# Performance work log

Measured on AMD Instinct MI355X. Metric: run time of the kernel, lower is better.

Reference implementation:

```python
import jax, jax.numpy as jnp
import numpy as np

N = 50000   # nodes
E = 800000  # edges
C = 64      # node feature channels (0e)
A = 4       # edge attr channels
B = 16      # edge embedding (radial basis) size
H = 8       # radial MLP hidden size
D = 32      # query/key channels
P = 16      # node attr channels
R_MAX = 5.0


def setup_inputs() -> dict:
    key = jax.random.key(0)
    ks = jax.random.split(key, 20)
    w = lambda k, shape, fan_in: (jax.random.normal(k, shape, jnp.float32) / np.sqrt(fan_in).astype(np.float32))
    inp = {
        "node_feats": jax.random.normal(ks[0], (N, C), jnp.float32),
        "node_attrs": jax.random.normal(ks[1], (N, P), jnp.float32),
        "edge_embedding": jax.random.uniform(ks[2], (E, B), jnp.float32),
        "edge_attrs": jax.random.normal(ks[3], (E, A), jnp.float32),
        "positions": jax.random.normal(ks[4], (N, 3), jnp.float32) * 0.3,  # keep lengths < r_max
        "edge_src": jax.random.randint(ks[5], (E,), 0, N),
        "edge_dst": jax.random.randint(ks[6], (E,), 0, N),
        # parameters
        "W_q": w(ks[7], (C, D), C),            # h_q Linear
        "W1_k": w(ks[8], (B, H), B),           # radial MLP for tp_k
        "W2_k": w(ks[9], (H, C * A), H),
        "W1_v": w(ks[10], (B, H), B),          # radial MLP for tp_v
        "W2_v": w(ks[11], (H, C * A), H),
        "W_lin_k": w(ks[12], (C, D), C),       # linear_k
        "W_lin_v": w(ks[13], (C, C), C),       # linear_v
        "W_dot": w(ks[14], (D, D), D * D),     # FullyConnectedTensorProduct(q,k,'0e')
        "W_sc": w(ks[15], (C, P, C), C * P),   # self connection FCTP
    }
    return inp


def soft_unit_step(x):
    safe = jnp.where(x > 0, x, 1.0)
    return jnp.where(x > 0, jnp.exp(-1.0 / safe), 0.0)


def uvu_tp(x_src, edge_attrs, edge_embedding, W1, W2):
    # radial MLP -> per-edge, per-path weights [E, C, A]; 'uvu' tensor product on scalars
    wgt = (jax.nn.silu(edge_embedding @ W1) @ W2).reshape(-1, C, A)
    return x_src * (jnp.einsum('eca,ea->ec', wgt, edge_attrs) / np.sqrt(A).astype(np.float32))


def reference(node_feats, node_attrs, edge_embedding, edge_attrs, positions,
              edge_src, edge_dst, W_q, W1_k, W2_k, W1_v, W2_v,
              W_lin_k, W_lin_v, W_dot, W_sc):
    q = (node_feats @ W_q)[edge_dst]                              # [E, D]
    x_src = node_feats[edge_src]                                  # [E, C]
    k = uvu_tp(x_src, edge_attrs, edge_embedding, W1_k, W2_k) @ W_lin_k  # [E, D]
    v = uvu_tp(x_src, edge_attrs, edge_embedding, W1_v, W2_v) @ W_lin_v  # [E, C]

    edge_vec = positions[edge_dst] - positions[edge_src]
    edge_length = jnp.linalg.norm(edge_vec, axis=1)               # [E]
    cutoff = soft_unit_step(2.0 * R_MAX * (1.0 - edge_length / R_MAX))

    score = jnp.einsum('ei,ij,ej->e', q, W_dot, k)                # weighted bilinear dot -> 0e
    expv = cutoff * jnp.exp(score)                                # [E]
    z = jax.ops.segment_sum(expv, edge_dst, num_segments=N)       # softmax normalizer
    z = jnp.where(z == 0, 1.0, z)
    alpha = expv / z[edge_dst]
    msg = jnp.sqrt(jax.nn.relu(alpha))[:, None] * v               # [E, C]
    node_out = jax.ops.segment_sum(msg, edge_dst, num_segments=N)  # [N, C]

    sc = jnp.einsum('nc,np,cpo->no', node_feats, node_attrs, W_sc)
    return node_out + sc
```

## Files before the change

kernel.cpp:

```cpp
#include <hip/hip_runtime.h>
#include <math.h>

#define NN 50000
#define EE 800000
#define NPAD 50176

typedef __attribute__((ext_vector_type(8))) short short8v;
typedef __attribute__((ext_vector_type(4))) float f32x4;

static __device__ __forceinline__ short bf16r(float x) {
  union { float f; unsigned u; } v; v.f = x;
  unsigned r = v.u + 0x7FFFu + ((v.u >> 16) & 1u);
  return (short)(r >> 16);
}
static __device__ __forceinline__ float bf2f(unsigned u) {
  union { unsigned u; float f; } v; v.u = u << 16;
  return v.f;
}
static __device__ __forceinline__ unsigned pk2(float a, float b) {
  return (unsigned)(unsigned short)bf16r(a) | ((unsigned)(unsigned short)bf16r(b) << 16);
}


__global__ __launch_bounds__(256) void prep_kernel(
    const float* __restrict__ Wq, const float* __restrict__ Wdot,
    const float* __restrict__ Wlk, const float* __restrict__ W2k,
    const float* __restrict__ W2v, const float* __restrict__ Wlv,
    const float* __restrict__ Wsc, float* __restrict__ M,
    unsigned short* __restrict__ w2kT, unsigned short* __restrict__ w2vT,
    unsigned short* __restrict__ wlvb, unsigned short* __restrict__ wscb,
    int* __restrict__ cur, int* __restrict__ bsum)
{
  const int tid = threadIdx.x;
  const int b = blockIdx.x;
  if (b == 0) {
    __shared__ float tmp[2048];
#pragma unroll
    for (int r = 0; r < 8; ++r) {
      int idx = tid + r * 256;
      int cin = idx >> 5, d = idx & 31;
      float a = 0.f;
      for (int j = 0; j < 32; ++j) a = fmaf(Wq[cin * 32 + j], Wdot[j * 32 + d], a);
      tmp[idx] = a;
    }
    __syncthreads();
#pragma unroll
    for (int r = 0; r < 16; ++r) {
      int idx = tid + r * 256;
      int cin = idx >> 6, c = idx & 63;
      float a = 0.f;
      for (int d = 0; d < 32; ++d) a = fmaf(tmp[cin * 32 + d], Wlk[c * 32 + d], a);
      M[idx] = a;
    }
#pragma unroll
    for (int r = 0; r < 8; ++r) {
      int idx = tid + r * 256;
      int c = idx >> 5, k = idx & 31, h = k >> 2, a = k & 3;
      w2kT[idx] = (unsigned short)bf16r(W2k[h * 256 + c * 4 + a]);
      w2vT[idx] = (unsigned short)bf16r(W2v[h * 256 + c * 4 + a]);
    }
#pragma unroll
    for (int r = 0; r < 16; ++r) {
      int idx = tid + r * 256;
      int o = idx >> 6, c = idx & 63;
      wlvb[idx] = (unsigned short)bf16r(Wlv[c * 64 + o]);
    }
  } else if (b <= 196) {
    cur[(b - 1) * 256 + tid] = 0;
    if (b == 1 && tid == 0) bsum[255] = 0;
  } else {
    int w = (b - 197) * 256 + tid;
    int c = w & 63, o = (w >> 6) & 63, p = w >> 12;
    wscb[w] = (unsigned short)bf16r(Wsc[c * 1024 + p * 64 + o]);
  }
}

__global__ __launch_bounds__(256) void tqhist_kernel(
    const float* __restrict__ nf, const float* __restrict__ M,
    const int* __restrict__ edst, int* __restrict__ cur,
    float4* __restrict__ zu,
    unsigned short* __restrict__ tqb, unsigned short* __restrict__ nfb)
{
  __shared__ float Ml[4096];
  __shared__ float nfl[64 * 68];
  const int tid = threadIdx.x;
  if (blockIdx.x < 3125) {
    int i = blockIdx.x * 256 + tid;
    float4 zf = make_float4(0.f, 0.f, 0.f, 0.f);
    zu[i] = zf;
    if (i < 12544) zu[800000 + i] = zf;
    atomicAdd(&cur[edst[i]], 1);
    return;
  }
  const int base = (blockIdx.x - 3125) * 64;
#pragma unroll
  for (int r = 0; r < 4; ++r) {
    int idx = tid + r * 256;
    reinterpret_cast<float4*>(Ml)[idx] = reinterpret_cast<const float4*>(M)[idx];
  }
#pragma unroll
  for (int r = 0; r < 4; ++r) {
    int idx = tid + r * 256;
    int row = idx >> 4, c4 = idx & 15;
    float4 v = make_float4(0.f, 0.f, 0.f, 0.f);
    if (base + row < NN) v = reinterpret_cast<const float4*>(nf)[(base + row) * 16 + c4];
    *reinterpret_cast<float4*>(&nfl[row * 68 + c4 * 4]) = v;
  }
  __syncthreads();
  const int to = tid & 15, tn = tid >> 4;
  float4 acc[4] = {make_float4(0,0,0,0), make_float4(0,0,0,0),
                   make_float4(0,0,0,0), make_float4(0,0,0,0)};
  for (int c = 0; c < 64; ++c) {
    float4 m = reinterpret_cast<const float4*>(Ml)[c * 16 + to];
#pragma unroll
    for (int i = 0; i < 4; ++i) {
      float x = nfl[(tn * 4 + i) * 68 + c];
      acc[i].x = fmaf(x, m.x, acc[i].x);
      acc[i].y = fmaf(x, m.y, acc[i].y);
      acc[i].z = fmaf(x, m.z, acc[i].z);
      acc[i].w = fmaf(x, m.w, acc[i].w);
    }
  }
#pragma unroll
  for (int i = 0; i < 4; ++i) {
    int n = base + tn * 4 + i;
    if (n < NN) {
      unsigned* tp = reinterpret_cast<unsigned*>(tqb) + (size_t)n * 32 + to * 2;
      tp[0] = pk2(acc[i].x, acc[i].y);
      tp[1] = pk2(acc[i].z, acc[i].w);
    }
  }
#pragma unroll
  for (int r = 0; r < 8; ++r) {
    int idx = tid + r * 256;
    int row = idx >> 5, cp = idx & 31;
    int n = base + row;
    if (n < NN) {
      reinterpret_cast<unsigned*>(nfb)[(size_t)n * 32 + cp] =
          pk2(nfl[row * 68 + cp * 2], nfl[row * 68 + cp * 2 + 1]);
    }
  }
}

__global__ __launch_bounds__(256) void scanAB_kernel(
    int* __restrict__ cur, int* __restrict__ bsum)
{
  __shared__ int s[256];
  __shared__ int isLast;
  const int tid = threadIdx.x;
  const int i = blockIdx.x * 256 + tid;
  int v = cur[i];
  s[tid] = v;
  __syncthreads();
  for (int off = 1; off < 256; off <<= 1) {
    int t = (tid >= off) ? s[tid - off] : 0;
    __syncthreads();
    s[tid] += t;
    __syncthreads();
  }
  cur[i] = s[tid] - v;
  if (tid == 255) bsum[blockIdx.x] = s[255];
  __threadfence();
  if (tid == 0) isLast = (atomicAdd(&bsum[255], 1) == 195);
  __syncthreads();
  if (!isLast) return;
  int v2 = (tid < 196) ? atomicAdd(&bsum[tid], 0) : 0;
  s[tid] = v2;
  __syncthreads();
  for (int off = 1; off < 256; off <<= 1) {
    int t = (tid >= off) ? s[tid - off] : 0;
    __syncthreads();
    s[tid] += t;
    __syncthreads();
  }
  if (tid < 196) bsum[tid] = s[tid] - v2;
}

__global__ __launch_bounds__(256) void scatter_fused(
    const int* __restrict__ esrc, const int* __restrict__ edst,
    const float* __restrict__ ea, const float* __restrict__ eb,
    const float* __restrict__ pos, const float* __restrict__ W1k,
    const float* __restrict__ W1v, int* __restrict__ cur,
    const int* __restrict__ bsum, int* __restrict__ perm,
    float* __restrict__ rec)
{
  int e = blockIdx.x * 256 + threadIdx.x;
  int s = esrc[e], d = edst[e];
  int r = atomicAdd(&cur[d], 1) + bsum[d >> 8];
  perm[r] = e;
  float dx = pos[d * 3 + 0] - pos[s * 3 + 0];
  float dy = pos[d * 3 + 1] - pos[s * 3 + 1];
  float dz = pos[d * 3 + 2] - pos[s * 3 + 2];
  float len = sqrtf(fmaf(dx, dx, fmaf(dy, dy, dz * dz)));
  float arg = 10.f - 2.f * len;
  float cl = (arg > 0.f) ? __expf(-1.f / arg) : 0.f;
  const f32x4* eb4 = reinterpret_cast<const f32x4*>(eb);
  f32x4 q0 = eb4[e * 4 + 0], q1 = eb4[e * 4 + 1],
        q2 = eb4[e * 4 + 2], q3 = eb4[e * 4 + 3];
  float ebv[16] = {q0.x, q0.y, q0.z, q0.w, q1.x, q1.y, q1.z, q1.w,
                   q2.x, q2.y, q2.z, q2.w, q3.x, q3.y, q3.z, q3.w};
  float h[16];
#pragma unroll
  for (int j = 0; j < 16; ++j) h[j] = 0.f;
#pragma unroll
  for (int b = 0; b < 16; ++b) {
    float x = ebv[b];
#pragma unroll
    for (int j = 0; j < 8; ++j) {
      h[j]     = fmaf(x, W1k[b * 8 + j], h[j]);
      h[8 + j] = fmaf(x, W1v[b * 8 + j], h[8 + j]);
    }
  }
#pragma unroll
  for (int j = 0; j < 16; ++j) h[j] = h[j] / (1.f + __expf(-h[j]));

  f32x4 a4 = reinterpret_cast<const f32x4*>(ea)[e];
  f32x4* rp4 = reinterpret_cast<f32x4*>(rec + (size_t)e * 12);
  f32x4 w0, w1, w2;
  w0.x = cl;
  w0.y = __uint_as_float(pk2(a4.x, a4.y));
  w0.z = __uint_as_float(pk2(a4.z, a4.w));
  w0.w = 0.f;
  w1.x = __uint_as_float(pk2(h[0], h[1]));
  w1.y = __uint_as_float(pk2(h[8], h[9]));
  w1.z = __uint_as_float(pk2(h[2], h[3]));
  w1.w = __uint_as_float(pk2(h[10], h[11]));
  w2.x = __uint_as_float(pk2(h[4], h[5]));
  w2.y = __uint_as_float(pk2(h[12], h[13]));
  w2.z = __uint_as_float(pk2(h[6], h[7]));
  w2.w = __uint_as_float(pk2(h[14], h[15]));
  rp4[0] = w0;
  rp4[1] = w1;
  rp4[2] = w2;
}

__global__ __launch_bounds__(256) void edge_kernel(
    const unsigned short* __restrict__ nfb, const unsigned short* __restrict__ tqb,
    const float* __restrict__ rec, const int* __restrict__ perm,
    const int* __restrict__ esrc, const int* __restrict__ edst,
    const unsigned short* __restrict__ w2kT, const unsigned short* __restrict__ w2vT,
    float* __restrict__ z, float* __restrict__ U)
{
  __shared__ float xsAll[4][16 * 68];
  __shared__ int   esAll[4][16];
  __shared__ int   edAll[4][16];
  __shared__ float clAll[4][16];
  __shared__ float evAll[4][16];
  const int tid  = threadIdx.x;
  const int lane = tid & 63;
  const int w = tid >> 6;
  const int lo = lane & 15, hi = lane >> 4;
  const int sb = (blockIdx.x * 4 + w) * 16;
  float* xs = xsAll[w];
  int*   es = esAll[w];
  int*   ed = edAll[w];
  float* cl = clAll[w];
  float* evs = evAll[w];

  short8v bk[4], bv[4];
#pragma unroll
  for (int t = 0; t < 4; ++t) {
    bk[t] = *reinterpret_cast<const short8v*>(&w2kT[(16 * t + lo) * 32 + hi * 8]);
    bv[t] = *reinterpret_cast<const short8v*>(&w2vT[(16 * t + lo) * 32 + hi * 8]);
  }

  const int eL = perm[sb + lo];
  const unsigned* ru = reinterpret_cast<const unsigned*>(rec);
  const size_t rb = (size_t)eL * 12;
  unsigned ea01 = ru[rb + 1];
  unsigned ea23 = ru[rb + 2];
  uint2 kv = *reinterpret_cast<const uint2*>(&ru[rb + 4 + 2 * hi]);
  unsigned k01 = kv.x, v01 = kv.y;
  if (hi == 0) {
    es[lo] = esrc[eL];
    ed[lo] = edst[eL];
    cl[lo] = rec[rb];
  }
  __builtin_amdgcn_wave_barrier();

#pragma unroll
  for (int r = 0; r < 2; ++r) {
    int idx = lane + r * 64;
    int e = idx >> 3, c8 = idx & 7;
    float4 pv = reinterpret_cast<const float4*>(nfb)[(size_t)es[e] * 8 + c8];
    unsigned u0 = __float_as_uint(pv.x), u1 = __float_as_uint(pv.y),
             u2 = __float_as_uint(pv.z), u3 = __float_as_uint(pv.w);
    float* xp = &xs[e * 68 + c8 * 8];
    xp[0] = bf2f(u0 & 0xffffu); xp[1] = bf2f(u0 >> 16);
    xp[2] = bf2f(u1 & 0xffffu); xp[3] = bf2f(u1 >> 16);
    xp[4] = bf2f(u2 & 0xffffu); xp[5] = bf2f(u2 >> 16);
    xp[6] = bf2f(u3 & 0xffffu); xp[7] = bf2f(u3 >> 16);
  }

  float ax = bf2f(ea01 & 0xffffu), ay = bf2f(ea01 >> 16);
  float az = bf2f(ea23 & 0xffffu), aw = bf2f(ea23 >> 16);
  float hk0 = bf2f(k01 & 0xffffu), hk1 = bf2f(k01 >> 16);
  float hv0 = bf2f(v01 & 0xffffu), hv1 = bf2f(v01 >> 16);
  short8v ak, av;
  ak[0] = bf16r(hk0 * ax); ak[1] = bf16r(hk0 * ay);
  ak[2] = bf16r(hk0 * az); ak[3] = bf16r(hk0 * aw);
  ak[4] = bf16r(hk1 * ax); ak[5] = bf16r(hk1 * ay);
  ak[6] = bf16r(hk1 * az); ak[7] = bf16r(hk1 * aw);
  av[0] = bf16r(hv0 * ax); av[1] = bf16r(hv0 * ay);
  av[2] = bf16r(hv0 * az); av[3] = bf16r(hv0 * aw);
  av[4] = bf16r(hv1 * ax); av[5] = bf16r(hv1 * ay);
  av[6] = bf16r(hv1 * az); av[7] = bf16r(hv1 * aw);
  __builtin_amdgcn_wave_barrier();

  f32x4 zero = {0.f, 0.f, 0.f, 0.f};
  f32x4 ack[4], acv[4];
#pragma unroll
  for (int t = 0; t < 4; ++t) {
    ack[t] = __builtin_amdgcn_mfma_f32_16x16x32_bf16(ak, bk[t], zero, 0, 0, 0);
    acv[t] = __builtin_amdgcn_mfma_f32_16x16x32_bf16(av, bv[t], zero, 0, 0, 0);
  }

  const int erow = 4 * hi;
  const unsigned short* tp0 = tqb + (size_t)ed[erow + 0] * 64;
  const unsigned short* tp1 = tqb + (size_t)ed[erow + 1] * 64;
  const unsigned short* tp2 = tqb + (size_t)ed[erow + 2] * 64;
  const unsigned short* tp3 = tqb + (size_t)ed[erow + 3] * 64;
  float p0 = 0.f, p1 = 0.f, p2 = 0.f, p3 = 0.f;
#pragma unroll
  for (int t = 0; t < 4; ++t) {
    int c = lo + 16 * t;
    p0 = fmaf(xs[(erow + 0) * 68 + c] * bf2f(tp0[c]), ack[t][0], p0);
    p1 = fmaf(xs[(erow + 1) * 68 + c] * bf2f(tp1[c]), ack[t][1], p1);
    p2 = fmaf(xs[(erow + 2) * 68 + c] * bf2f(tp2[c]), ack[t][2], p2);
    p3 = fmaf(xs[(erow + 3) * 68 + c] * bf2f(tp3[c]), ack[t][3], p3);
  }
#pragma unroll
  for (int off = 1; off < 16; off <<= 1) {
    p0 += __shfl_xor(p0, off);
    p1 += __shfl_xor(p1, off);
    p2 += __shfl_xor(p2, off);
    p3 += __shfl_xor(p3, off);
  }
  float ev0 = cl[erow + 0] * __expf(0.5f * p0);
  float ev1 = cl[erow + 1] * __expf(0.5f * p1);
  float ev2 = cl[erow + 2] * __expf(0.5f * p2);
  float ev3 = cl[erow + 3] * __expf(0.5f * p3);
  float se0 = sqrtf(ev0), se1 = sqrtf(ev1), se2 = sqrtf(ev2), se3 = sqrtf(ev3);
  if (lo < 4) {
    float ev = (lo == 0) ? ev0 : (lo == 1) ? ev1 : (lo == 2) ? ev2 : ev3;
    evs[erow + lo] = ev;
  }
#pragma unroll
  for (int i = 0; i < 4; ++i) {
    const float se = (i == 0) ? se0 : (i == 1) ? se1 : (i == 2) ? se2 : se3;
    float* xr = &xs[(erow + i) * 68 + lo];
#pragma unroll
    for (int t = 0; t < 4; ++t) {
      xr[16 * t] = se * xr[16 * t] * acv[t][i];
    }
  }
  __builtin_amdgcn_wave_barrier();
  {
    const int c = lane;
    float acc = 0.f, evacc = 0.f;
    int prev = ed[0];
#pragma unroll
    for (int r = 0; r < 16; ++r) {
      int d = ed[r];
      if (d != prev) {
        unsafeAtomicAdd(&U[prev * 64 + c], acc);
        if (c == 0) unsafeAtomicAdd(&z[prev], evacc);
        acc = 0.f; evacc = 0.f; prev = d;
      }
      acc += xs[r * 68 + c];
      if (c == 0) evacc += evs[r];
    }
    unsafeAtomicAdd(&U[prev * 64 + c], acc);
    if (c == 0) unsafeAtomicAdd(&z[prev], evacc);
  }
}

__global__ __launch_bounds__(256, 4) void final_kernel(
    const float* __restrict__ nf, const float* __restrict__ na,
    const float* __restrict__ U, const float* __restrict__ z,
    const unsigned short* __restrict__ wscb, const unsigned short* __restrict__ wlvb,
    float* __restrict__ out)
{
  __shared__ float nfl[64 * 68];
  __shared__ float Ul[64 * 68];
  __shared__ float nal[64 * 17];
  __shared__ float sl[64];
  const int tid = threadIdx.x;
  const int lane = tid & 63;
  const int lo = lane & 15, hi = lane >> 4;
  const int w = tid >> 6;
  const int nb = blockIdx.x * 64;

#pragma unroll
  for (int r = 0; r < 4; ++r) {
    int idx = tid + r * 256;
    int row = idx >> 4, c4 = idx & 15;
    int n = nb + row; if (n >= NN) n = NN - 1;
    float4 v = reinterpret_cast<const float4*>(nf)[n * 16 + c4];
    *reinterpret_cast<float4*>(&nfl[row * 68 + c4 * 4]) = v;
    float4 u = reinterpret_cast<const float4*>(U)[n * 16 + c4];
    *reinterpret_cast<float4*>(&Ul[row * 68 + c4 * 4]) = u;
  }
#pragma unroll
  for (int r = 0; r < 4; ++r) {
    int idx = tid + r * 256;
    int row = idx >> 4, p = idx & 15;
    int n = nb + row; if (n >= NN) n = NN - 1;
    nal[row * 17 + p] = na[n * 16 + p];
  }
  if (tid < 64) {
    int n = nb + tid; if (n >= NN) n = NN - 1;
    float zz = z[n];
    sl[tid] = (zz > 0.f) ? 0.5f * rsqrtf(zz) : 0.f;
  }
  __syncthreads();

  const int row = 16 * w + lo;
  short8v anf[2], au[2];
#pragma unroll
  for (int kk = 0; kk < 2; ++kk) {
#pragma unroll
    for (int j = 0; j < 8; ++j) {
      anf[kk][j] = bf16r(nfl[row * 68 + 32 * kk + 8 * hi + j]);
      au[kk][j]  = bf16r(Ul[row * 68 + 32 * kk + 8 * hi + j]);
    }
  }

  f32x4 zeroA = {0.f, 0.f, 0.f, 0.f};
  f32x4 accS[4] = {zeroA, zeroA, zeroA, zeroA};
  f32x4 accU[4] = {zeroA, zeroA, zeroA, zeroA};

#pragma unroll
  for (int t = 0; t < 4; ++t) {
    short8v b0 = *reinterpret_cast<const short8v*>(&wlvb[(16 * t + lo) * 64 + 8 * hi]);
    short8v b1 = *reinterpret_cast<const short8v*>(&wlvb[(16 * t + lo) * 64 + 32 + 8 * hi]);
    accU[t] = __builtin_amdgcn_mfma_f32_16x16x32_bf16(au[0], b0, accU[t], 0, 0, 0);
    accU[t] = __builtin_amdgcn_mfma_f32_16x16x32_bf16(au[1], b1, accU[t], 0, 0, 0);
  }
#pragma unroll 1
  for (int p = 0; p < 16; ++p) {
    f32x4 cp[4] = {zeroA, zeroA, zeroA, zeroA};
#pragma unroll
    for (int t = 0; t < 4; ++t) {
      const int bbase = (p * 64 + 16 * t + lo) * 64 + 8 * hi;
      short8v b0 = *reinterpret_cast<const short8v*>(&wscb[bbase]);
      short8v b1 = *reinterpret_cast<const short8v*>(&wscb[bbase + 32]);
      cp[t] = __builtin_amdgcn_mfma_f32_16x16x32_bf16(anf[0], b0, cp[t], 0, 0, 0);
      cp[t] = __builtin_amdgcn_mfma_f32_16x16x32_bf16(anf[1], b1, cp[t], 0, 0, 0);
    }
#pragma unroll
    for (int i = 0; i < 4; ++i) {
      float nav = nal[(16 * w + 4 * hi + i) * 17 + p];
#pragma unroll
      for (int t = 0; t < 4; ++t) accS[t][i] = fmaf(nav, cp[t][i], accS[t][i]);
    }
  }
#pragma unroll
  for (int i = 0; i < 4; ++i) {
    int n = nb + 16 * w + 4 * hi + i;
    if (n < NN) {
      float s = sl[16 * w + 4 * hi + i];
#pragma unroll
      for (int t = 0; t < 4; ++t) {
        out[n * 64 + 16 * t + lo] = fmaf(s, accU[t][i], accS[t][i]);
      }
    }
  }
}

extern "C" void kernel_launch(void* const* d_in, const int* in_sizes, int n_in,
                              void* d_out, int out_size, void* d_ws, size_t ws_size,
                              hipStream_t stream) {
  const float* nf   = (const float*)d_in[0];
  const float* na   = (const float*)d_in[1];
  const float* eb   = (const float*)d_in[2];
  const float* ea   = (const float*)d_in[3];
  const float* pos  = (const float*)d_in[4];
  const int*   esrc = (const int*)d_in[5];
  const int*   edst = (const int*)d_in[6];
  const float* Wq   = (const float*)d_in[7];
  const float* W1k  = (const float*)d_in[8];
  const float* W2k  = (const float*)d_in[9];
  const float* W1v  = (const float*)d_in[10];
  const float* W2v  = (const float*)d_in[11];
  const float* Wlk  = (const float*)d_in[12];
  const float* Wlv  = (const float*)d_in[13];
  const float* Wdot = (const float*)d_in[14];
  const float* Wsc  = (const float*)d_in[15];
  float* out = (float*)d_out;

  float* wsf = (float*)d_ws;
  float* z    = wsf;
  float* U    = wsf + 50176;
  unsigned short* nfb = (unsigned short*)(wsf + 3250176);
  unsigned short* tqb = (unsigned short*)(wsf + 4850176);
  unsigned short* w2kT = (unsigned short*)(wsf + 6450176);
  unsigned short* w2vT = (unsigned short*)(wsf + 6451200);
  unsigned short* wlvb = (unsigned short*)(wsf + 6452224);
  unsigned short* wscb = (unsigned short*)(wsf + 6454272);
  int*   cur  = (int*)(wsf + 6487040);
  int*   bsum = (int*)(wsf + 6537216);
  float* M    = wsf + 6537472;
  float* rec  = wsf + 6541568;
  int*   perm = (int*)(wsf + 16141568);

  prep_kernel<<<453, 256, 0, stream>>>(Wq, Wdot, Wlk, W2k, W2v, Wlv, Wsc,
                                       M, w2kT, w2vT, wlvb, wscb, cur, bsum);
  tqhist_kernel<<<3907, 256, 0, stream>>>(nf, M, edst, cur, (float4*)z, tqb, nfb);
  scanAB_kernel<<<196, 256, 0, stream>>>(cur, bsum);
  scatter_fused<<<EE / 256, 256, 0, stream>>>(esrc, edst, ea, eb, pos, W1k, W1v,
                                              cur, bsum, perm, rec);
  edge_kernel<<<EE / 64, 256, 0, stream>>>(nfb, tqb, rec, perm, esrc, edst,
                                           w2kT, w2vT, z, U);
  final_kernel<<<(NN + 63) / 64, 256, 0, stream>>>(nf, na, U, z, wscb, wlvb, out);
}
```

Before: 314.4 us.

## Fuse radial MLP and cutoff into edge kernel, drop packed edge record

```diff
diff --git a/kernel.cpp b/kernel.cpp
--- a/kernel.cpp
+++ b/kernel.cpp
@@ -176,68 +176,22 @@
   if (tid < 196) bsum[tid] = s[tid] - v2;
 }
 
-__global__ __launch_bounds__(256) void scatter_fused(
-    const int* __restrict__ esrc, const int* __restrict__ edst,
-    const float* __restrict__ ea, const float* __restrict__ eb,
-    const float* __restrict__ pos, const float* __restrict__ W1k,
-    const float* __restrict__ W1v, int* __restrict__ cur,
-    const int* __restrict__ bsum, int* __restrict__ perm,
-    float* __restrict__ rec)
+__global__ __launch_bounds__(256) void perm_scatter(
+    const int* __restrict__ edst, int* __restrict__ cur,
+    const int* __restrict__ bsum, int* __restrict__ perm)
 {
   int e = blockIdx.x * 256 + threadIdx.x;
-  int s = esrc[e], d = edst[e];
+  int d = edst[e];
   int r = atomicAdd(&cur[d], 1) + bsum[d >> 8];
   perm[r] = e;
-  float dx = pos[d * 3 + 0] - pos[s * 3 + 0];
-  float dy = pos[d * 3 + 1] - pos[s * 3 + 1];
-  float dz = pos[d * 3 + 2] - pos[s * 3 + 2];
-  float len = sqrtf(fmaf(dx, dx, fmaf(dy, dy, dz * dz)));
-  float arg = 10.f - 2.f * len;
-  float cl = (arg > 0.f) ? __expf(-1.f / arg) : 0.f;
-  const f32x4* eb4 = reinterpret_cast<const f32x4*>(eb);
-  f32x4 q0 = eb4[e * 4 + 0], q1 = eb4[e * 4 + 1],
-        q2 = eb4[e * 4 + 2], q3 = eb4[e * 4 + 3];
-  float ebv[16] = {q0.x, q0.y, q0.z, q0.w, q1.x, q1.y, q1.z, q1.w,
-                   q2.x, q2.y, q2.z, q2.w, q3.x, q3.y, q3.z, q3.w};
-  float h[16];
-#pragma unroll
-  for (int j = 0; j < 16; ++j) h[j] = 0.f;
-#pragma unroll
-  for (int b = 0; b < 16; ++b) {
-    float x = ebv[b];
-#pragma unroll
-    for (int j = 0; j < 8; ++j) {
-      h[j]     = fmaf(x, W1k[b * 8 + j], h[j]);
-      h[8 + j] = fmaf(x, W1v[b * 8 + j], h[8 + j]);
-    }
-  }
-#pragma unroll
-  for (int j = 0; j < 16; ++j) h[j] = h[j] / (1.f + __expf(-h[j]));
-
-  f32x4 a4 = reinterpret_cast<const f32x4*>(ea)[e];
-  f32x4* rp4 = reinterpret_cast<f32x4*>(rec + (size_t)e * 12);
-  f32x4 w0, w1, w2;
-  w0.x = cl;
-  w0.y = __uint_as_float(pk2(a4.x, a4.y));
-  w0.z = __uint_as_float(pk2(a4.z, a4.w));
-  w0.w = 0.f;
-  w1.x = __uint_as_float(pk2(h[0], h[1]));
-  w1.y = __uint_as_float(pk2(h[8], h[9]));
-  w1.z = __uint_as_float(pk2(h[2], h[3]));
-  w1.w = __uint_as_float(pk2(h[10], h[11]));
-  w2.x = __uint_as_float(pk2(h[4], h[5]));
-  w2.y = __uint_as_float(pk2(h[12], h[13]));
-  w2.z = __uint_as_float(pk2(h[6], h[7]));
-  w2.w = __uint_as_float(pk2(h[14], h[15]));
-  rp4[0] = w0;
-  rp4[1] = w1;
-  rp4[2] = w2;
 }
 
 __global__ __launch_bounds__(256) void edge_kernel(
     const unsigned short* __restrict__ nfb, const unsigned short* __restrict__ tqb,
-    const float* __restrict__ rec, const int* __restrict__ perm,
-    const int* __restrict__ esrc, const int* __restrict__ edst,
+    const int* __restrict__ perm, const int* __restrict__ esrc,
+    const int* __restrict__ edst, const float* __restrict__ ea,
+    const float* __restrict__ eb, const float* __restrict__ pos,
+    const float* __restrict__ W1k, const float* __restrict__ W1v,
     const unsigned short* __restrict__ w2kT, const unsigned short* __restrict__ w2vT,
     float* __restrict__ z, float* __restrict__ U)
 {
@@ -265,16 +219,16 @@
   }
 
   const int eL = perm[sb + lo];
-  const unsigned* ru = reinterpret_cast<const unsigned*>(rec);
-  const size_t rb = (size_t)eL * 12;
-  unsigned ea01 = ru[rb + 1];
-  unsigned ea23 = ru[rb + 2];
-  uint2 kv = *reinterpret_cast<const uint2*>(&ru[rb + 4 + 2 * hi]);
-  unsigned k01 = kv.x, v01 = kv.y;
+  const f32x4* eb4 = reinterpret_cast<const f32x4*>(eb);
+  f32x4 q0 = eb4[(size_t)eL * 4 + 0], q1 = eb4[(size_t)eL * 4 + 1],
+        q2 = eb4[(size_t)eL * 4 + 2], q3 = eb4[(size_t)eL * 4 + 3];
+  f32x4 a4 = reinterpret_cast<const f32x4*>(ea)[eL];
+  int sN = 0, dN = 0;
   if (hi == 0) {
-    es[lo] = esrc[eL];
-    ed[lo] = edst[eL];
-    cl[lo] = rec[rb];
+    sN = esrc[eL];
+    dN = edst[eL];
+    es[lo] = sN;
+    ed[lo] = dN;
   }
   __builtin_amdgcn_wave_barrier();
 
@@ -292,19 +246,40 @@
     xp[6] = bf2f(u3 & 0xffffu); xp[7] = bf2f(u3 >> 16);
   }
 
-  float ax = bf2f(ea01 & 0xffffu), ay = bf2f(ea01 >> 16);
-  float az = bf2f(ea23 & 0xffffu), aw = bf2f(ea23 >> 16);
-  float hk0 = bf2f(k01 & 0xffffu), hk1 = bf2f(k01 >> 16);
-  float hv0 = bf2f(v01 & 0xffffu), hv1 = bf2f(v01 >> 16);
+  float ebv[16] = {q0.x, q0.y, q0.z, q0.w, q1.x, q1.y, q1.z, q1.w,
+                   q2.x, q2.y, q2.z, q2.w, q3.x, q3.y, q3.z, q3.w};
+  float hk0 = 0.f, hk1 = 0.f, hv0 = 0.f, hv1 = 0.f;
+#pragma unroll
+  for (int b = 0; b < 16; ++b) {
+    float x = ebv[b];
+    float2 wk = *reinterpret_cast<const float2*>(W1k + b * 8 + 2 * hi);
+    float2 wv = *reinterpret_cast<const float2*>(W1v + b * 8 + 2 * hi);
+    hk0 = fmaf(x, wk.x, hk0); hk1 = fmaf(x, wk.y, hk1);
+    hv0 = fmaf(x, wv.x, hv0); hv1 = fmaf(x, wv.y, hv1);
+  }
+  hk0 = hk0 / (1.f + __expf(-hk0));
+  hk1 = hk1 / (1.f + __expf(-hk1));
+  hv0 = hv0 / (1.f + __expf(-hv0));
+  hv1 = hv1 / (1.f + __expf(-hv1));
+
+  if (hi == 0) {
+    float dx = pos[dN * 3 + 0] - pos[sN * 3 + 0];
+    float dy = pos[dN * 3 + 1] - pos[sN * 3 + 1];
+    float dz = pos[dN * 3 + 2] - pos[sN * 3 + 2];
+    float len = sqrtf(fmaf(dx, dx, fmaf(dy, dy, dz * dz)));
+    float arg = 10.f - 2.f * len;
+    cl[lo] = (arg > 0.f) ? __expf(-1.f / arg) : 0.f;
+  }
+
   short8v ak, av;
-  ak[0] = bf16r(hk0 * ax); ak[1] = bf16r(hk0 * ay);
-  ak[2] = bf16r(hk0 * az); ak[3] = bf16r(hk0 * aw);
-  ak[4] = bf16r(hk1 * ax); ak[5] = bf16r(hk1 * ay);
-  ak[6] = bf16r(hk1 * az); ak[7] = bf16r(hk1 * aw);
-  av[0] = bf16r(hv0 * ax); av[1] = bf16r(hv0 * ay);
-  av[2] = bf16r(hv0 * az); av[3] = bf16r(hv0 * aw);
-  av[4] = bf16r(hv1 * ax); av[5] = bf16r(hv1 * ay);
-  av[6] = bf16r(hv1 * az); av[7] = bf16r(hv1 * aw);
+  ak[0] = bf16r(hk0 * a4.x); ak[1] = bf16r(hk0 * a4.y);
+  ak[2] = bf16r(hk0 * a4.z); ak[3] = bf16r(hk0 * a4.w);
+  ak[4] = bf16r(hk1 * a4.x); ak[5] = bf16r(hk1 * a4.y);
+  ak[6] = bf16r(hk1 * a4.z); ak[7] = bf16r(hk1 * a4.w);
+  av[0] = bf16r(hv0 * a4.x); av[1] = bf16r(hv0 * a4.y);
+  av[2] = bf16r(hv0 * a4.z); av[3] = bf16r(hv0 * a4.w);
+  av[4] = bf16r(hv1 * a4.x); av[5] = bf16r(hv1 * a4.y);
+  av[6] = bf16r(hv1 * a4.z); av[7] = bf16r(hv1 * a4.w);
   __builtin_amdgcn_wave_barrier();
 
   f32x4 zero = {0.f, 0.f, 0.f, 0.f};
@@ -501,16 +476,14 @@
   int*   cur  = (int*)(wsf + 6487040);
   int*   bsum = (int*)(wsf + 6537216);
   float* M    = wsf + 6537472;
-  float* rec  = wsf + 6541568;
-  int*   perm = (int*)(wsf + 16141568);
+  int*   perm = (int*)(wsf + 6541568);
 
   prep_kernel<<<453, 256, 0, stream>>>(Wq, Wdot, Wlk, W2k, W2v, Wlv, Wsc,
                                        M, w2kT, w2vT, wlvb, wscb, cur, bsum);
   tqhist_kernel<<<3907, 256, 0, stream>>>(nf, M, edst, cur, (float4*)z, tqb, nfb);
   scanAB_kernel<<<196, 256, 0, stream>>>(cur, bsum);
-  scatter_fused<<<EE / 256, 256, 0, stream>>>(esrc, edst, ea, eb, pos, W1k, W1v,
-                                              cur, bsum, perm, rec);
-  edge_kernel<<<EE / 64, 256, 0, stream>>>(nfb, tqb, rec, perm, esrc, edst,
-                                           w2kT, w2vT, z, U);
+  perm_scatter<<<EE / 256, 256, 0, stream>>>(edst, cur, bsum, perm);
+  edge_kernel<<<EE / 64, 256, 0, stream>>>(nfb, tqb, perm, esrc, edst, ea, eb, pos,
+                                           W1k, W1v, w2kT, w2vT, z, U);
   final_kernel<<<(NN + 63) / 64, 256, 0, stream>>>(nf, na, U, z, wscb, wlvb, out);
 }
```

New measurement: 369.6 us. 17.6% more time.
